# Performance work log

Hardware: AMD Instinct MI355X
Metric: run time of the kernel (lower is better)

## Reference

```python
import jax, jax.numpy as jnp
import numpy as np

EPS = 1e-6

def setup_inputs() -> dict:
    key = jax.random.key(0)
    k1, k2, k3 = jax.random.split(key, 3)
    B, N, F, OUT = 16, 1024, 64, 128
    x = jax.random.normal(k1, (B, N, F), dtype=jnp.float32)
    A = jax.random.uniform(k2, (B, N, N), dtype=jnp.float32)
    kernel = jax.random.normal(k3, (3 * F, OUT), dtype=jnp.float32) * 0.05
    bias = jnp.zeros((OUT,), dtype=jnp.float32)
    return {"x": x, "A": A, "kernel": kernel, "bias": bias}


def reference(x, A, kernel, bias):
    # x: [B,N,F], A: [B,N,N]
    n = A.shape[-1]
    eye = jnp.eye(n, dtype=A.dtype)
    Az = A * (1.0 - eye)          # zero out diagonal (A -= diag(diag_part(A)))
    A_hat = Az + eye              # add self-loops
    deg = A_hat.sum(axis=2)       # [B,N]
    inv_asym = 1.0 / (EPS + deg)                 # D^{-1}
    s = 1.0 / (EPS + jnp.sqrt(deg))              # D^{-1/2}
    # Three message-passing variants; apply diagonal scalings as broadcasts
    o1 = jnp.matmul(Az, x)                                   # A x
    o2 = inv_asym[:, :, None] * jnp.matmul(A_hat, x)         # D^{-1} A_hat x
    o3 = s[:, :, None] * jnp.matmul(A_hat, s[:, :, None] * x)  # D^{-1/2} A_hat D^{-1/2} x
    out = jnp.concatenate([o1, o2, o3], axis=-1)             # [B,N,3F]
    out = jnp.matmul(out, kernel) + bias                     # [B,N,OUT]
    return jax.nn.relu(out)
```

## Files before the change

### kernel.cpp

```cpp
#include <hip/hip_runtime.h>
#include <hip/hip_bf16.h>
#include <cstdint>

#define BATCH 16
#define NN    1024
#define FF    64
#define OUTF  128
#define KCAT  192
#define EPSV  1e-6f

typedef __attribute__((ext_vector_type(4))) float  f32x4;
typedef __attribute__((ext_vector_type(8))) __bf16 bf16x8;
typedef __attribute__((ext_vector_type(4))) __bf16 bf16x4;

__global__ __launch_bounds__(256) void k_deg_cvt(const float* __restrict__ A,
                                                 float* __restrict__ d1,
                                                 float* __restrict__ sArr,
                                                 __bf16* __restrict__ Az) {
    int wave = threadIdx.x >> 6;
    int lane = threadIdx.x & 63;
    int row  = blockIdx.x * 4 + wave;
    int i    = row & (NN - 1);
    const f32x4* rp = (const f32x4*)(A + (size_t)row * NN);
    __bf16* op = Az + (size_t)row * NN;
    float sum = 0.f;
#pragma unroll
    for (int t = 0; t < 4; ++t) {
        f32x4 v = rp[t * 64 + lane];
        int base = (t * 64 + lane) * 4;
#pragma unroll
        for (int q = 0; q < 4; ++q)
            if (base + q == i) v[q] = 0.f;
        sum += v[0] + v[1] + v[2] + v[3];
        bf16x4 o;
#pragma unroll
        for (int q = 0; q < 4; ++q) o[q] = (__bf16)v[q];
        *(bf16x4*)(op + base) = o;
    }
#pragma unroll
    for (int off = 32; off; off >>= 1) sum += __shfl_xor(sum, off);
    if (lane == 0) {
        float deg = 1.0f + sum;
        d1[row]   = 1.0f / (EPSV + deg);
        sArr[row] = 1.0f / (EPSV + sqrtf(deg));
    }
}

__global__ __launch_bounds__(256) void k_prep(const float* __restrict__ x,
                                              const float* __restrict__ sArr,
                                              const float* __restrict__ kern,
                                              __bf16* __restrict__ xT,
                                              __bf16* __restrict__ sxT,
                                              __bf16* __restrict__ KT) {
    __shared__ float tile[64][65];
    int bid = blockIdx.x;
    int b   = bid >> 4;
    int k0  = (bid & 15) * 64;
    const float* xp = x + ((size_t)b * NN + k0) * FF;
    for (int i = threadIdx.x; i < 64 * 64; i += 256) {
        int r = i >> 6, c = i & 63;
        tile[r][c] = xp[r * FF + c];
    }
    __syncthreads();
    for (int i = threadIdx.x; i < 64 * 64; i += 256) {
        int c = i >> 6, kk = i & 63;
        float v  = tile[kk][c];
        float sv = v * sArr[b * NN + k0 + kk];
        size_t o = ((size_t)b * FF + c) * NN + k0 + kk;
        xT[o]  = (__bf16)v;
        sxT[o] = (__bf16)sv;
    }
    if (threadIdx.x < 96) {
        int idx = bid * 96 + threadIdx.x;
        int c = idx / KCAT;
        int k = idx - c * KCAT;
        KT[idx] = (__bf16)kern[k * OUTF + c];
    }
}

__global__ __launch_bounds__(128) void k_main(const __bf16* __restrict__ Az,
                                              const float* __restrict__ x,
                                              const float* __restrict__ bias,
                                              const float* __restrict__ d1g,
                                              const float* __restrict__ sg,
                                              const __bf16* __restrict__ xT,
                                              const __bf16* __restrict__ sxT,
                                              const __bf16* __restrict__ KT,
                                              float* __restrict__ out) {
    __shared__ __align__(16) __bf16 os[16][208];

    const int tid  = threadIdx.x;
    const int ch   = tid >> 6;
    const int lane = tid & 63;
    const int l15  = lane & 15;
    const int h8   = (lane >> 4) * 8;
    const int bid  = blockIdx.x;
    const int b    = bid >> 6;
    const int row0 = (bid & 63) * 16;

    const __bf16* aP  = Az  + ((size_t)(b * NN + row0 + l15)) * NN + h8;
    const __bf16* xP0 = xT  + ((size_t)(b * FF + ch * 32 + l15)) * NN + h8;
    const __bf16* xP1 = xT  + ((size_t)(b * FF + ch * 32 + 16 + l15)) * NN + h8;
    const __bf16* sP0 = sxT + ((size_t)(b * FF + ch * 32 + l15)) * NN + h8;
    const __bf16* sP1 = sxT + ((size_t)(b * FF + ch * 32 + 16 + l15)) * NN + h8;

    f32x4 P0 = {}, P1 = {}, Q0 = {}, Q1 = {};

    bf16x8 aA, x0A, x1A, s0A, s1A;
    bf16x8 aB, x0B, x1B, s0B, s1B;
    bf16x8 aC, x0C, x1C, s0C, s1C;
    bf16x8 aD, x0D, x1D, s0D, s1D;

#define LOADSET(S, tt)                                          \
    a##S  = *(const bf16x8*)(aP  + (tt) * 32);                  \
    x0##S = *(const bf16x8*)(xP0 + (tt) * 32);                  \
    x1##S = *(const bf16x8*)(xP1 + (tt) * 32);                  \
    s0##S = *(const bf16x8*)(sP0 + (tt) * 32);                  \
    s1##S = *(const bf16x8*)(sP1 + (tt) * 32);

#define COMPUTE(S)                                                          \
    P0 = __builtin_amdgcn_mfma_f32_16x16x32_bf16(a##S, x0##S, P0, 0, 0, 0); \
    P1 = __builtin_amdgcn_mfma_f32_16x16x32_bf16(a##S, x1##S, P1, 0, 0, 0); \
    Q0 = __builtin_amdgcn_mfma_f32_16x16x32_bf16(a##S, s0##S, Q0, 0, 0, 0); \
    Q1 = __builtin_amdgcn_mfma_f32_16x16x32_bf16(a##S, s1##S, Q1, 0, 0, 0);

    LOADSET(A, 0)
    LOADSET(B, 1)
    LOADSET(C, 2)
    LOADSET(D, 3)
#pragma unroll
    for (int t = 0; t < 32; t += 4) {
        COMPUTE(A) if (t + 4 < 32) { LOADSET(A, t + 4) }
        COMPUTE(B) if (t + 5 < 32) { LOADSET(B, t + 5) }
        COMPUTE(C) if (t + 6 < 32) { LOADSET(C, t + 6) }
        COMPUTE(D) if (t + 7 < 32) { LOADSET(D, t + 7) }
    }
#undef LOADSET
#undef COMPUTE

#pragma unroll
    for (int j = 0; j < 4; ++j) {
        int rr   = (lane >> 4) * 4 + j;
        int grow = b * NN + row0 + rr;
        float dv = d1g[grow];
        float sv = sg[grow];
        {
            int cc = ch * 32 + l15;
            float xv = x[(size_t)grow * FF + cc];
            os[rr][cc]       = (__bf16)P0[j];
            os[rr][64 + cc]  = (__bf16)(dv * (P0[j] + xv));
            os[rr][128 + cc] = (__bf16)(sv * (Q0[j] + sv * xv));
        }
        {
            int cc = ch * 32 + 16 + l15;
            float xv = x[(size_t)grow * FF + cc];
            os[rr][cc]       = (__bf16)P1[j];
            os[rr][64 + cc]  = (__bf16)(dv * (P1[j] + xv));
            os[rr][128 + cc] = (__bf16)(sv * (Q1[j] + sv * xv));
        }
    }
    __syncthreads();

    f32x4 acc0 = {}, acc1 = {}, acc2 = {}, acc3 = {};
    const int orow = l15;
#pragma unroll
    for (int ks = 0; ks < 6; ++ks) {
        bf16x8 of = *(const bf16x8*)&os[orow][ks * 32 + h8];
        bf16x8 k0 = *(const bf16x8*)&KT[(size_t)(ch * 64 + 0  + l15) * KCAT + ks * 32 + h8];
        bf16x8 k1 = *(const bf16x8*)&KT[(size_t)(ch * 64 + 16 + l15) * KCAT + ks * 32 + h8];
        bf16x8 k2 = *(const bf16x8*)&KT[(size_t)(ch * 64 + 32 + l15) * KCAT + ks * 32 + h8];
        bf16x8 k3 = *(const bf16x8*)&KT[(size_t)(ch * 64 + 48 + l15) * KCAT + ks * 32 + h8];
        acc0 = __builtin_amdgcn_mfma_f32_16x16x32_bf16(of, k0, acc0, 0, 0, 0);
        acc1 = __builtin_amdgcn_mfma_f32_16x16x32_bf16(of, k1, acc1, 0, 0, 0);
        acc2 = __builtin_amdgcn_mfma_f32_16x16x32_bf16(of, k2, acc2, 0, 0, 0);
        acc3 = __builtin_amdgcn_mfma_f32_16x16x32_bf16(of, k3, acc3, 0, 0, 0);
    }
#pragma unroll
    for (int cg = 0; cg < 4; ++cg) {
        f32x4 av = cg == 0 ? acc0 : cg == 1 ? acc1 : cg == 2 ? acc2 : acc3;
        int col  = ch * 64 + cg * 16 + l15;
        float bv = bias[col];
#pragma unroll
        for (int j = 0; j < 4; ++j) {
            int rr  = (lane >> 4) * 4 + j;
            float v = av[j] + bv;
            out[((size_t)b * NN + row0 + rr) * OUTF + col] = v > 0.f ? v : 0.f;
        }
    }
}

extern "C" void kernel_launch(void* const* d_in, const int* in_sizes, int n_in,
                              void* d_out, int out_size, void* d_ws, size_t ws_size,
                              hipStream_t stream) {
    const float* x    = (const float*)d_in[0];
    const float* A    = (const float*)d_in[1];
    const float* kern = (const float*)d_in[2];
    const float* bias = (const float*)d_in[3];
    float* out = (float*)d_out;

    char* ws = (char*)d_ws;
    __bf16* Az  = (__bf16*)(ws);
    float*  d1  = (float*)(ws + 33554432);
    float*  s   = (float*)(ws + 33554432 + 65536);
    __bf16* xT  = (__bf16*)(ws + 33554432 + 131072);
    __bf16* sxT = (__bf16*)(ws + 33554432 + 131072 + 2097152);
    __bf16* KT  = (__bf16*)(ws + 33554432 + 131072 + 2 * 2097152);
    (void)ws_size; (void)in_sizes; (void)n_in; (void)out_size;

    k_deg_cvt<<<dim3(4096), dim3(256), 0, stream>>>(A, d1, s, Az);
    k_prep<<<dim3(256), dim3(256), 0, stream>>>(x, s, kern, xT, sxT, KT);
    k_main<<<dim3(1024), dim3(128), 0, stream>>>(Az, x, bias, d1, s, xT, sxT, KT, out);
}
```

Before: 153.8 us.

## Stage Az tile in LDS via direct global-to-LDS loads with split-K waves

The main kernel now handles 32 rows per block with 512 threads. It stages the 32x1024 bf16 Az tile into 64KB of LDS using global_load_lds, so each A fragment is read from global memory once and shared across the waves. The K dimension is split across two wave halves, and their partial sums are reduced through LDS. The blocks are also remapped to interleave batches. This cuts redundant global reads of the x/sx operands per row, but it serialises the full tile load before compute with no pipelining, and the large LDS use limits occupancy.

```diff
diff --git a/kernel.cpp b/kernel.cpp
--- a/kernel.cpp
+++ b/kernel.cpp
@@ -2,7 +2,6 @@
 #include <hip/hip_bf16.h>
 #include <cstdint>
 
-#define BATCH 16
 #define NN    1024
 #define FF    64
 #define OUTF  128
@@ -12,6 +11,12 @@
 typedef __attribute__((ext_vector_type(4))) float  f32x4;
 typedef __attribute__((ext_vector_type(8))) __bf16 bf16x8;
 typedef __attribute__((ext_vector_type(4))) __bf16 bf16x4;
+
+#define MFMA16(a, b, c) __builtin_amdgcn_mfma_f32_16x16x32_bf16(a, b, c, 0, 0, 0)
+#define GLOAD_LDS16(g, l)                                          \
+    __builtin_amdgcn_global_load_lds(                              \
+        (const __attribute__((address_space(1))) void*)(g),        \
+        (__attribute__((address_space(3))) void*)(l), 16, 0, 0)
 
 __global__ __launch_bounds__(256) void k_deg_cvt(const float* __restrict__ A,
                                                  float* __restrict__ d1,
@@ -78,113 +83,116 @@
     }
 }
 
-__global__ __launch_bounds__(128) void k_main(const __bf16* __restrict__ Az,
-                                              const float* __restrict__ x,
-                                              const float* __restrict__ bias,
-                                              const float* __restrict__ d1g,
-                                              const float* __restrict__ sg,
-                                              const __bf16* __restrict__ xT,
-                                              const __bf16* __restrict__ sxT,
-                                              const __bf16* __restrict__ KT,
-                                              float* __restrict__ out) {
-    __shared__ __align__(16) __bf16 os[16][208];
+__global__ __launch_bounds__(512, 4) void k_main(const __bf16* __restrict__ Az,
+                                                 const float* __restrict__ x,
+                                                 const float* __restrict__ bias,
+                                                 const float* __restrict__ d1g,
+                                                 const float* __restrict__ sg,
+                                                 const __bf16* __restrict__ xT,
+                                                 const __bf16* __restrict__ sxT,
+                                                 const __bf16* __restrict__ KT,
+                                                 float* __restrict__ out) {
+    __shared__ __align__(16) char smem[65536];
 
     const int tid  = threadIdx.x;
-    const int ch   = tid >> 6;
+    const int w    = tid >> 6;
     const int lane = tid & 63;
     const int l15  = lane & 15;
     const int h8   = (lane >> 4) * 8;
-    const int bid  = blockIdx.x;
-    const int b    = bid >> 6;
-    const int row0 = (bid & 63) * 16;
-
-    const __bf16* aP  = Az  + ((size_t)(b * NN + row0 + l15)) * NN + h8;
-    const __bf16* xP0 = xT  + ((size_t)(b * FF + ch * 32 + l15)) * NN + h8;
-    const __bf16* xP1 = xT  + ((size_t)(b * FF + ch * 32 + 16 + l15)) * NN + h8;
-    const __bf16* sP0 = sxT + ((size_t)(b * FF + ch * 32 + l15)) * NN + h8;
-    const __bf16* sP1 = sxT + ((size_t)(b * FF + ch * 32 + 16 + l15)) * NN + h8;
+
+    const int work = (blockIdx.x & 7) * 64 + (blockIdx.x >> 3);
+    const int b    = work >> 5;
+    const int row0 = (work & 31) * 32;
+
+    {
+        const __bf16* AzB = Az + (size_t)(b * NN + row0) * NN;
+        int rgl  = (tid >> 6) & 1;
+        int rowL = rgl * 16 + (tid & 15);
+        int colB = ((tid >> 7) * 32) + (((tid >> 4) & 3) * 8);
+        const __bf16* src = AzB + (size_t)rowL * NN + colB;
+        char* ldsb = smem + ((tid >> 6) << 10);
+#pragma unroll
+        for (int c = 0; c < 8; ++c)
+            GLOAD_LDS16(src + c * 128, ldsb + c * 8192);
+    }
+
+    const int h  = w >> 2;
+    const int cw = w & 3;
+
+    const __bf16* xP = xT  + ((size_t)(b * FF + cw * 16 + l15)) * NN + h * 512 + h8;
+    const __bf16* sP = sxT + ((size_t)(b * FF + cw * 16 + l15)) * NN + h * 512 + h8;
+    const char* ldsA = smem + h * 32768 + lane * 16;
+
+    asm volatile("s_waitcnt vmcnt(0)" ::: "memory");
+    __syncthreads();
 
     f32x4 P0 = {}, P1 = {}, Q0 = {}, Q1 = {};
-
-    bf16x8 aA, x0A, x1A, s0A, s1A;
-    bf16x8 aB, x0B, x1B, s0B, s1B;
-    bf16x8 aC, x0C, x1C, s0C, s1C;
-    bf16x8 aD, x0D, x1D, s0D, s1D;
-
-#define LOADSET(S, tt)                                          \
-    a##S  = *(const bf16x8*)(aP  + (tt) * 32);                  \
-    x0##S = *(const bf16x8*)(xP0 + (tt) * 32);                  \
-    x1##S = *(const bf16x8*)(xP1 + (tt) * 32);                  \
-    s0##S = *(const bf16x8*)(sP0 + (tt) * 32);                  \
-    s1##S = *(const bf16x8*)(sP1 + (tt) * 32);
-
-#define COMPUTE(S)                                                          \
-    P0 = __builtin_amdgcn_mfma_f32_16x16x32_bf16(a##S, x0##S, P0, 0, 0, 0); \
-    P1 = __builtin_amdgcn_mfma_f32_16x16x32_bf16(a##S, x1##S, P1, 0, 0, 0); \
-    Q0 = __builtin_amdgcn_mfma_f32_16x16x32_bf16(a##S, s0##S, Q0, 0, 0, 0); \
-    Q1 = __builtin_amdgcn_mfma_f32_16x16x32_bf16(a##S, s1##S, Q1, 0, 0, 0);
-
-    LOADSET(A, 0)
-    LOADSET(B, 1)
-    LOADSET(C, 2)
-    LOADSET(D, 3)
-#pragma unroll
-    for (int t = 0; t < 32; t += 4) {
-        COMPUTE(A) if (t + 4 < 32) { LOADSET(A, t + 4) }
-        COMPUTE(B) if (t + 5 < 32) { LOADSET(B, t + 5) }
-        COMPUTE(C) if (t + 6 < 32) { LOADSET(C, t + 6) }
-        COMPUTE(D) if (t + 7 < 32) { LOADSET(D, t + 7) }
-    }
-#undef LOADSET
-#undef COMPUTE
-
-#pragma unroll
-    for (int j = 0; j < 4; ++j) {
-        int rr   = (lane >> 4) * 4 + j;
-        int grow = b * NN + row0 + rr;
-        float dv = d1g[grow];
-        float sv = sg[grow];
-        {
-            int cc = ch * 32 + l15;
-            float xv = x[(size_t)grow * FF + cc];
-            os[rr][cc]       = (__bf16)P0[j];
-            os[rr][64 + cc]  = (__bf16)(dv * (P0[j] + xv));
-            os[rr][128 + cc] = (__bf16)(sv * (Q0[j] + sv * xv));
+#pragma unroll
+    for (int tt = 0; tt < 16; ++tt) {
+        bf16x8 a0 = *(const bf16x8*)(ldsA + tt * 2048);
+        bf16x8 a1 = *(const bf16x8*)(ldsA + tt * 2048 + 1024);
+        bf16x8 xf = *(const bf16x8*)(xP + tt * 32);
+        bf16x8 sf = *(const bf16x8*)(sP + tt * 32);
+        P0 = MFMA16(a0, xf, P0);
+        P1 = MFMA16(a1, xf, P1);
+        Q0 = MFMA16(a0, sf, Q0);
+        Q1 = MFMA16(a1, sf, Q1);
+    }
+
+    __syncthreads();
+    f32x4* sp = (f32x4*)(smem + 32768 + cw * 4096);
+    if (h == 1) {
+        sp[lane]       = P0;
+        sp[lane + 64]  = P1;
+        sp[lane + 128] = Q0;
+        sp[lane + 192] = Q1;
+    }
+    __syncthreads();
+    __bf16 (*os)[208] = (__bf16(*)[208])smem;
+    if (h == 0) {
+        P0 += sp[lane];  P1 += sp[lane + 64];
+        Q0 += sp[lane + 128];  Q1 += sp[lane + 192];
+#pragma unroll
+        for (int rg = 0; rg < 2; ++rg) {
+            f32x4 Pv = rg ? P1 : P0;
+            f32x4 Qv = rg ? Q1 : Q0;
+#pragma unroll
+            for (int j = 0; j < 4; ++j) {
+                int rr   = rg * 16 + (lane >> 4) * 4 + j;
+                int grow = b * NN + row0 + rr;
+                float dv = d1g[grow];
+                float sv = sg[grow];
+                int cc   = cw * 16 + l15;
+                float xv = x[(size_t)grow * FF + cc];
+                os[rr][cc]        = (__bf16)Pv[j];
+                os[rr][64 + cc]   = (__bf16)(dv * (Pv[j] + xv));
+                os[rr][128 + cc]  = (__bf16)(sv * (Qv[j] + sv * xv));
+            }
         }
-        {
-            int cc = ch * 32 + 16 + l15;
-            float xv = x[(size_t)grow * FF + cc];
-            os[rr][cc]       = (__bf16)P1[j];
-            os[rr][64 + cc]  = (__bf16)(dv * (P1[j] + xv));
-            os[rr][128 + cc] = (__bf16)(sv * (Q1[j] + sv * xv));
-        }
-    }
-    __syncthreads();
-
-    f32x4 acc0 = {}, acc1 = {}, acc2 = {}, acc3 = {};
-    const int orow = l15;
+    }
+    __syncthreads();
+
+    const int rge = w >> 2;
+    const int cg2 = w & 3;
+    f32x4 e0 = {}, e1 = {};
 #pragma unroll
     for (int ks = 0; ks < 6; ++ks) {
-        bf16x8 of = *(const bf16x8*)&os[orow][ks * 32 + h8];
-        bf16x8 k0 = *(const bf16x8*)&KT[(size_t)(ch * 64 + 0  + l15) * KCAT + ks * 32 + h8];
-        bf16x8 k1 = *(const bf16x8*)&KT[(size_t)(ch * 64 + 16 + l15) * KCAT + ks * 32 + h8];
-        bf16x8 k2 = *(const bf16x8*)&KT[(size_t)(ch * 64 + 32 + l15) * KCAT + ks * 32 + h8];
-        bf16x8 k3 = *(const bf16x8*)&KT[(size_t)(ch * 64 + 48 + l15) * KCAT + ks * 32 + h8];
-        acc0 = __builtin_amdgcn_mfma_f32_16x16x32_bf16(of, k0, acc0, 0, 0, 0);
-        acc1 = __builtin_amdgcn_mfma_f32_16x16x32_bf16(of, k1, acc1, 0, 0, 0);
-        acc2 = __builtin_amdgcn_mfma_f32_16x16x32_bf16(of, k2, acc2, 0, 0, 0);
-        acc3 = __builtin_amdgcn_mfma_f32_16x16x32_bf16(of, k3, acc3, 0, 0, 0);
-    }
-#pragma unroll
-    for (int cg = 0; cg < 4; ++cg) {
-        f32x4 av = cg == 0 ? acc0 : cg == 1 ? acc1 : cg == 2 ? acc2 : acc3;
-        int col  = ch * 64 + cg * 16 + l15;
+        bf16x8 of = *(const bf16x8*)&os[rge * 16 + l15][ks * 32 + h8];
+        bf16x8 k0 = *(const bf16x8*)&KT[(size_t)(cg2 * 32 + l15) * KCAT + ks * 32 + h8];
+        bf16x8 k1 = *(const bf16x8*)&KT[(size_t)(cg2 * 32 + 16 + l15) * KCAT + ks * 32 + h8];
+        e0 = MFMA16(of, k0, e0);
+        e1 = MFMA16(of, k1, e1);
+    }
+#pragma unroll
+    for (int g = 0; g < 2; ++g) {
+        f32x4 ev = g ? e1 : e0;
+        int col  = cg2 * 32 + g * 16 + l15;
         float bv = bias[col];
 #pragma unroll
         for (int j = 0; j < 4; ++j) {
-            int rr  = (lane >> 4) * 4 + j;
-            float v = av[j] + bv;
-            out[((size_t)b * NN + row0 + rr) * OUTF + col] = v > 0.f ? v : 0.f;
+            int rr  = rge * 16 + (lane >> 4) * 4 + j;
+            float v = ev[j] + bv;
+            out[((size_t)(b * NN + row0 + rr)) * OUTF + col] = v > 0.f ? v : 0.f;
         }
     }
 }
@@ -209,5 +217,5 @@
 
     k_deg_cvt<<<dim3(4096), dim3(256), 0, stream>>>(A, d1, s, Az);
     k_prep<<<dim3(256), dim3(256), 0, stream>>>(x, s, kern, xT, sxT, KT);
-    k_main<<<dim3(1024), dim3(128), 0, stream>>>(Az, x, bias, d1, s, xT, sxT, KT, out);
-}
+    k_main<<<dim3(512), dim3(512), 0, stream>>>(Az, x, bias, d1, s, xT, sxT, KT, out);
+}
```

After: 138.0 us. 10.3% less time.
